# Kernel tuning notes

Measured on AMD Instinct MI355X. Metric: run time of the kernel, lower is better.

## Reference

```python
import jax, jax.numpy as jnp
import numpy as np

GAMMA = 1.0


def setup_inputs() -> dict:
    key = jax.random.key(0)
    kx, ky = jax.random.split(key)
    x = jax.random.normal(kx, (8192, 128), dtype=jnp.float32)
    y = jax.random.normal(ky, (8192, 128), dtype=jnp.float32)
    return {"x": x, "y": y}


def reference(x, y):
    # RBF kernel K[i,j] = exp(-gamma * ||x_i - y_j||^2)
    x2 = jnp.sum(x * x, axis=1)              # [N]
    y2 = jnp.sum(y * y, axis=1)              # [M]
    xy = jnp.einsum('nd,md->nm', x, y)       # [N, M] GEMM
    sq = x2[:, None] + y2[None, :] - 2.0 * xy
    sq = jnp.maximum(sq, 0.0)                # guard tiny negatives from cancellation
    return jnp.exp(-GAMMA * sq)
```

## Files before the change

### kernel.cpp

```cpp
#include <hip/hip_runtime.h>
#include <hip/hip_bf16.h>

typedef __bf16 bf16x8 __attribute__((ext_vector_type(8)));
typedef float f32x4 __attribute__((ext_vector_type(4)));
typedef unsigned short us4 __attribute__((ext_vector_type(4)));

#define TILE 128
#define APAD 136
#define OPAD 132

__device__ __forceinline__ unsigned short f2bf(float f) {
    unsigned u = __float_as_uint(f);
    u += 0x7fffu + ((u >> 16) & 1u);
    return (unsigned short)(u >> 16);
}
__device__ __forceinline__ float bf2f(unsigned short h) {
    return __uint_as_float(((unsigned)h) << 16);
}

__global__ __launch_bounds__(256, 2)
void rbf_mfma(const float* __restrict__ X, const float* __restrict__ Y,
              float* __restrict__ O, int ldo) {
    __shared__ __align__(16) char smem[70656];
    unsigned short* Ab  = (unsigned short*)smem;
    unsigned short* Bb  = (unsigned short*)(smem + 34816);
    float*          Ol  = (float*)smem;
    float*          x2s = (float*)(smem + 69632);
    float*          y2s = (float*)(smem + 70144);

    const int t    = threadIdx.x;
    const int row0 = blockIdx.x * TILE;
    const int col0 = blockIdx.y * TILE;
    const float* xs = X + (size_t)row0 * 128;
    const float* ys = Y + (size_t)col0 * 128;

#pragma unroll
    for (int i = 0; i < 16; ++i) {
        int idx = i * 256 + t;
        int r   = idx >> 5;
        int c   = (idx & 31) * 4;
        float4 a = ((const float4*)xs)[idx];
        float4 b = ((const float4*)ys)[idx];
        us4 av, bv;
        av.x = f2bf(a.x); av.y = f2bf(a.y); av.z = f2bf(a.z); av.w = f2bf(a.w);
        bv.x = f2bf(b.x); bv.y = f2bf(b.y); bv.z = f2bf(b.z); bv.w = f2bf(b.w);
        *(us4*)&Ab[r * APAD + c] = av;
        *(us4*)&Bb[r * APAD + c] = bv;
    }
    __syncthreads();

    {
        int r = t & 127;
        const unsigned short* src = (t < 128) ? Ab : Bb;
        float s = 0.f;
#pragma unroll
        for (int c = 0; c < 128; c += 4) {
            us4 v = *(const us4*)&src[r * APAD + c];
            float f0 = bf2f(v.x), f1 = bf2f(v.y), f2 = bf2f(v.z), f3 = bf2f(v.w);
            s += f0 * f0 + f1 * f1 + f2 * f2 + f3 * f3;
        }
        if (t < 128) x2s[r] = s; else y2s[r] = s;
    }
    __syncthreads();

    const int l  = t & 63;
    const int w  = t >> 6;
    const int wr = (w >> 1) * 64;
    const int wc = (w & 1) * 64;
    const int lr = l & 15;
    const int kg = (l >> 4) * 8;

    f32x4 acc[4][4] = {};
#pragma unroll
    for (int k0 = 0; k0 < 128; k0 += 32) {
        bf16x8 af[4], bfr[4];
#pragma unroll
        for (int m = 0; m < 4; ++m)
            af[m] = *(const bf16x8*)&Ab[(wr + m * 16 + lr) * APAD + k0 + kg];
#pragma unroll
        for (int n = 0; n < 4; ++n)
            bfr[n] = *(const bf16x8*)&Bb[(wc + n * 16 + lr) * APAD + k0 + kg];
#pragma unroll
        for (int m = 0; m < 4; ++m)
#pragma unroll
            for (int n = 0; n < 4; ++n)
                acc[m][n] = __builtin_amdgcn_mfma_f32_16x16x32_bf16(
                    af[m], bfr[n], acc[m][n], 0, 0, 0);
    }
    __syncthreads();

#pragma unroll
    for (int m = 0; m < 4; ++m) {
        int rb = wr + m * 16 + (l >> 4) * 4;
#pragma unroll
        for (int n = 0; n < 4; ++n) {
            int cc = wc + n * 16 + lr;
            float y2 = y2s[cc];
            f32x4 v = acc[m][n];
#pragma unroll
            for (int i = 0; i < 4; ++i) {
                float sq = x2s[rb + i] + y2 - 2.f * v[i];
                sq = fmaxf(sq, 0.f);
                Ol[(rb + i) * OPAD + cc] = __expf(-sq);
            }
        }
    }
    __syncthreads();

#pragma unroll
    for (int i = 0; i < 16; ++i) {
        int idx = i * 256 + t;
        int r   = idx >> 5;
        int c   = (idx & 31) * 4;
        *(float4*)&O[(size_t)(row0 + r) * ldo + col0 + c] =
            *(const float4*)&Ol[r * OPAD + c];
    }
}

extern "C" void kernel_launch(void* const* d_in, const int* in_sizes, int n_in,
                              void* d_out, int out_size, void* d_ws, size_t ws_size,
                              hipStream_t stream) {
    const float* X = (const float*)d_in[0];
    const float* Y = (const float*)d_in[1];
    float* O = (float*)d_out;
    const int N = in_sizes[0] / 128;
    const int M = in_sizes[1] / 128;
    dim3 grid(N / TILE, M / TILE);
    rbf_mfma<<<grid, dim3(256), 0, stream>>>(X, Y, O, M);
}
```

Baseline: 324.1 us.

## Precompute bf16 swizzled inputs and norms in prep kernel, direct LDS loads in main

Adds a prep kernel that converts X and Y to bf16 once, in a swizzled layout, and computes the fp32 row norms into workspace. The main kernel then loads tiles with global_load_lds straight into shared memory and reads them back with XOR-swizzled addressing. It writes the exp output directly from registers with nontemporal scalar stores instead of staging through LDS. This removes the conversion repeated by every tile and halves input bytes per tile, but adds a second launch, and the scalar stores may coalesce worse than the old float4 stores. Norms are now computed from fp32 values rather than from the bf16 copies.

```diff
diff --git a/kernel.cpp b/kernel.cpp
--- a/kernel.cpp
+++ b/kernel.cpp
@@ -5,115 +5,114 @@
 typedef float f32x4 __attribute__((ext_vector_type(4)));
 typedef unsigned short us4 __attribute__((ext_vector_type(4)));
 
-#define TILE 128
-#define APAD 136
-#define OPAD 132
-
 __device__ __forceinline__ unsigned short f2bf(float f) {
     unsigned u = __float_as_uint(f);
     u += 0x7fffu + ((u >> 16) & 1u);
     return (unsigned short)(u >> 16);
 }
-__device__ __forceinline__ float bf2f(unsigned short h) {
-    return __uint_as_float(((unsigned)h) << 16);
+
+__global__ __launch_bounds__(256)
+void rbf_prep(const float* __restrict__ X, const float* __restrict__ Y,
+              unsigned short* __restrict__ Xb, unsigned short* __restrict__ Yb,
+              float* __restrict__ x2, float* __restrict__ y2) {
+    const int b = blockIdx.x;
+    const float* src = (b < 128) ? X : Y;
+    unsigned short* db = (b < 128) ? Xb : Yb;
+    float* dn = (b < 128) ? x2 : y2;
+    const int r0 = (b & 127) * 64;
+    const int t = threadIdx.x;
+    const f32x4* s4 = (const f32x4*)(src + (size_t)r0 * 128);
+#pragma unroll
+    for (int i = 0; i < 8; ++i) {
+        int idx = i * 256 + t;
+        int r = idx >> 5, c4 = idx & 31;
+        f32x4 v = s4[idx];
+        us4 o;
+        o.x = f2bf(v[0]); o.y = f2bf(v[1]); o.z = f2bf(v[2]); o.w = f2bf(v[3]);
+        int pc = (c4 >> 1) ^ (r & 7);
+        *(us4*)&db[(size_t)(r0 + r) * 128 + pc * 8 + (c4 & 1) * 4] = o;
+    }
+    if (t < 64) {
+        const f32x4* row = (const f32x4*)(src + (size_t)(r0 + t) * 128);
+        float s = 0.f;
+#pragma unroll
+        for (int c = 0; c < 32; ++c) {
+            f32x4 v = row[c];
+            s += v[0] * v[0] + v[1] * v[1] + v[2] * v[2] + v[3] * v[3];
+        }
+        dn[r0 + t] = s;
+    }
 }
 
 __global__ __launch_bounds__(256, 2)
-void rbf_mfma(const float* __restrict__ X, const float* __restrict__ Y,
+void rbf_main(const unsigned short* __restrict__ Xb, const unsigned short* __restrict__ Yb,
+              const float* __restrict__ x2, const float* __restrict__ y2,
               float* __restrict__ O, int ldo) {
-    __shared__ __align__(16) char smem[70656];
-    unsigned short* Ab  = (unsigned short*)smem;
-    unsigned short* Bb  = (unsigned short*)(smem + 34816);
-    float*          Ol  = (float*)smem;
-    float*          x2s = (float*)(smem + 69632);
-    float*          y2s = (float*)(smem + 70144);
+    __shared__ __align__(16) unsigned short Ab[16384];
+    __shared__ __align__(16) unsigned short Bb[16384];
+    const int t = threadIdx.x, l = t & 63, w = t >> 6;
+    const int row0 = blockIdx.x * 128, col0 = blockIdx.y * 128;
 
-    const int t    = threadIdx.x;
-    const int row0 = blockIdx.x * TILE;
-    const int col0 = blockIdx.y * TILE;
-    const float* xs = X + (size_t)row0 * 128;
-    const float* ys = Y + (size_t)col0 * 128;
+    const char* gA = (const char*)(Xb + (size_t)row0 * 128);
+    const char* gB = (const char*)(Yb + (size_t)col0 * 128);
+#pragma unroll
+    for (int j = 0; j < 8; ++j) {
+        int base = (w * 8 + j) * 1024;
+        __builtin_amdgcn_global_load_lds(
+            (const __attribute__((address_space(1))) void*)(gA + base + l * 16),
+            (__attribute__((address_space(3))) void*)((char*)Ab + base), 16, 0, 0);
+        __builtin_amdgcn_global_load_lds(
+            (const __attribute__((address_space(1))) void*)(gB + base + l * 16),
+            (__attribute__((address_space(3))) void*)((char*)Bb + base), 16, 0, 0);
+    }
 
+    const int lr = l & 15, q = l >> 4;
+    const int wr = (w >> 1) * 64, wc = (w & 1) * 64;
+
+    f32x4 x2v[4]; float y2v[4];
 #pragma unroll
-    for (int i = 0; i < 16; ++i) {
-        int idx = i * 256 + t;
-        int r   = idx >> 5;
-        int c   = (idx & 31) * 4;
-        float4 a = ((const float4*)xs)[idx];
-        float4 b = ((const float4*)ys)[idx];
-        us4 av, bv;
-        av.x = f2bf(a.x); av.y = f2bf(a.y); av.z = f2bf(a.z); av.w = f2bf(a.w);
-        bv.x = f2bf(b.x); bv.y = f2bf(b.y); bv.z = f2bf(b.z); bv.w = f2bf(b.w);
-        *(us4*)&Ab[r * APAD + c] = av;
-        *(us4*)&Bb[r * APAD + c] = bv;
-    }
+    for (int m = 0; m < 4; ++m) x2v[m] = *(const f32x4*)&x2[row0 + wr + m * 16 + q * 4];
+#pragma unroll
+    for (int n = 0; n < 4; ++n) y2v[n] = y2[col0 + wc + n * 16 + lr];
+
     __syncthreads();
-
-    {
-        int r = t & 127;
-        const unsigned short* src = (t < 128) ? Ab : Bb;
-        float s = 0.f;
-#pragma unroll
-        for (int c = 0; c < 128; c += 4) {
-            us4 v = *(const us4*)&src[r * APAD + c];
-            float f0 = bf2f(v.x), f1 = bf2f(v.y), f2 = bf2f(v.z), f3 = bf2f(v.w);
-            s += f0 * f0 + f1 * f1 + f2 * f2 + f3 * f3;
-        }
-        if (t < 128) x2s[r] = s; else y2s[r] = s;
-    }
-    __syncthreads();
-
-    const int l  = t & 63;
-    const int w  = t >> 6;
-    const int wr = (w >> 1) * 64;
-    const int wc = (w & 1) * 64;
-    const int lr = l & 15;
-    const int kg = (l >> 4) * 8;
 
     f32x4 acc[4][4] = {};
 #pragma unroll
-    for (int k0 = 0; k0 < 128; k0 += 32) {
-        bf16x8 af[4], bfr[4];
+    for (int k = 0; k < 4; ++k) {
+        bf16x8 af[4], bv[4];
 #pragma unroll
-        for (int m = 0; m < 4; ++m)
-            af[m] = *(const bf16x8*)&Ab[(wr + m * 16 + lr) * APAD + k0 + kg];
+        for (int m = 0; m < 4; ++m) {
+            int R = wr + m * 16 + lr;
+            af[m] = *(const bf16x8*)((const char*)Ab + R * 256 + (((k << 2) + q) ^ (R & 7)) * 16);
+        }
 #pragma unroll
-        for (int n = 0; n < 4; ++n)
-            bfr[n] = *(const bf16x8*)&Bb[(wc + n * 16 + lr) * APAD + k0 + kg];
+        for (int n = 0; n < 4; ++n) {
+            int R = wc + n * 16 + lr;
+            bv[n] = *(const bf16x8*)((const char*)Bb + R * 256 + (((k << 2) + q) ^ (R & 7)) * 16);
+        }
 #pragma unroll
         for (int m = 0; m < 4; ++m)
 #pragma unroll
             for (int n = 0; n < 4; ++n)
-                acc[m][n] = __builtin_amdgcn_mfma_f32_16x16x32_bf16(
-                    af[m], bfr[n], acc[m][n], 0, 0, 0);
+                acc[m][n] = __builtin_amdgcn_mfma_f32_16x16x32_bf16(af[m], bv[n], acc[m][n], 0, 0, 0);
     }
-    __syncthreads();
 
 #pragma unroll
     for (int m = 0; m < 4; ++m) {
-        int rb = wr + m * 16 + (l >> 4) * 4;
+        int rbase = row0 + wr + m * 16 + q * 4;
 #pragma unroll
         for (int n = 0; n < 4; ++n) {
-            int cc = wc + n * 16 + lr;
-            float y2 = y2s[cc];
-            f32x4 v = acc[m][n];
+            float* op = &O[(size_t)rbase * ldo + col0 + wc + n * 16 + lr];
+            float yv = y2v[n];
 #pragma unroll
             for (int i = 0; i < 4; ++i) {
-                float sq = x2s[rb + i] + y2 - 2.f * v[i];
+                float sq = x2v[m][i] + yv - 2.0f * acc[m][n][i];
                 sq = fmaxf(sq, 0.f);
-                Ol[(rb + i) * OPAD + cc] = __expf(-sq);
+                __builtin_nontemporal_store(__expf(-sq), op);
+                op += ldo;
             }
         }
-    }
-    __syncthreads();
-
-#pragma unroll
-    for (int i = 0; i < 16; ++i) {
-        int idx = i * 256 + t;
-        int r   = idx >> 5;
-        int c   = (idx & 31) * 4;
-        *(float4*)&O[(size_t)(row0 + r) * ldo + col0 + c] =
-            *(const float4*)&Ol[r * OPAD + c];
     }
 }
 
@@ -125,6 +124,10 @@
     float* O = (float*)d_out;
     const int N = in_sizes[0] / 128;
     const int M = in_sizes[1] / 128;
-    dim3 grid(N / TILE, M / TILE);
-    rbf_mfma<<<grid, dim3(256), 0, stream>>>(X, Y, O, M);
+    unsigned short* Xb = (unsigned short*)d_ws;
+    unsigned short* Yb = Xb + (size_t)N * 128;
+    float* x2 = (float*)(Yb + (size_t)M * 128);
+    float* y2 = x2 + N;
+    rbf_prep<<<dim3((N + M) / 64), 256, 0, stream>>>(X, Y, Xb, Yb, x2, y2);
+    rbf_main<<<dim3(N / 128, M / 128), 256, 0, stream>>>(Xb, Yb, x2, y2, O, M);
 }
```

Result: faster. 314.2 us (-3.1%).
